# Optimization experiments

Hardware: AMD Instinct MI355X
Metric: run time of the kernel (lower is better)

## Reference

```python
import jax, jax.numpy as jnp
import numpy as np

D_MODEL = 512
NUM_HEADS = 8
D_K = D_MODEL // NUM_HEADS
DIM_FF = 2048
EPS = 1e-5


def layer_norm(x, gamma, beta):
    mu = jnp.mean(x, axis=-1, keepdims=True)
    var = jnp.mean(jnp.square(x - mu), axis=-1, keepdims=True)
    return (x - mu) * jax.lax.rsqrt(var + EPS) * gamma + beta


def setup_inputs() -> dict:
    key = jax.random.key(0)
    ks = jax.random.split(key, 10)
    B, L = 8, 1024
    s = 1.0 / np.sqrt(D_MODEL)
    return {
        "h": jax.random.normal(ks[0], (B, L, D_MODEL), jnp.float32),
        "attn_bias": jax.random.normal(ks[1], (B, NUM_HEADS, L, L), jnp.float32),
        "mask": jnp.ones((B, L), jnp.int32),
        "Wqkv": jax.random.normal(ks[2], (D_MODEL, 3 * D_MODEL), jnp.float32) * s,
        "bqkv": jnp.zeros((3 * D_MODEL,), jnp.float32),
        "Wo": jax.random.normal(ks[3], (D_MODEL, D_MODEL), jnp.float32) * s,
        "bo": jnp.zeros((D_MODEL,), jnp.float32),
        "W1": jax.random.normal(ks[4], (D_MODEL, DIM_FF), jnp.float32) * s,
        "b1": jnp.zeros((DIM_FF,), jnp.float32),
        "W2": jax.random.normal(ks[5], (DIM_FF, D_MODEL), jnp.float32) * (1.0 / np.sqrt(DIM_FF)),
        "b2": jnp.zeros((D_MODEL,), jnp.float32),
        "g1": jnp.ones((D_MODEL,), jnp.float32),
        "be1": jnp.zeros((D_MODEL,), jnp.float32),
        "g2": jnp.ones((D_MODEL,), jnp.float32),
        "be2": jnp.zeros((D_MODEL,), jnp.float32),
    }


def reference(h, attn_bias, mask, Wqkv, bqkv, Wo, bo, W1, b1, W2, b2, g1, be1, g2, be2):
    B, L, D = h.shape
    H, dk = NUM_HEADS, D_K
    qkv = h @ Wqkv + bqkv                      # [B, L, 3D]
    q, k, v = jnp.split(qkv, 3, axis=-1)
    q = q.reshape(B, L, H, dk).transpose(0, 2, 1, 3)  # [B, H, L, dk]
    k = k.reshape(B, L, H, dk).transpose(0, 2, 1, 3)
    v = v.reshape(B, L, H, dk).transpose(0, 2, 1, 3)
    scores = jnp.einsum('bhqd,bhkd->bhqk', q, k) / np.sqrt(dk)
    scores = scores + attn_bias
    scores = jnp.where(mask[:, None, None, :] > 0, scores, -jnp.inf)
    attn = jax.nn.softmax(scores, axis=-1)
    out = jnp.einsum('bhqk,bhkd->bhqd', attn, v)       # [B, H, L, dk]
    out = out.transpose(0, 2, 1, 3).reshape(B, L, D)
    out = out @ Wo + bo
    h = layer_norm(h + out, g1, be1)
    ff = jax.nn.relu(h @ W1 + b1) @ W2 + b2
    h = layer_norm(h + ff, g2, be2)
    return h
```

## Files before the change

### kernel.cpp

```cpp
#include <hip/hip_runtime.h>
#include <hip/hip_bf16.h>
#include <math.h>

#define NUM_HEADS 8
#define SEQ_L 1024
#define EPS 1e-5f
#define LOG2E 1.44269504088896f
#define KVB 128

typedef __bf16 bf16x8 __attribute__((ext_vector_type(8)));
typedef float f32x4 __attribute__((ext_vector_type(4)));
typedef __hip_bfloat16 bf16;

#define AS1 __attribute__((address_space(1)))
#define AS3 __attribute__((address_space(3)))

__device__ __forceinline__ void gload_lds16(const void* g, void* l) {
    __builtin_amdgcn_global_load_lds((const AS1 unsigned*)g, (AS3 unsigned*)l, 16, 0, 0);
}

__device__ __forceinline__ unsigned short bfb(float x) {
    bf16 b = __float2bfloat16(x);
    return *(unsigned short*)&b;
}

__device__ __forceinline__ int swz(int el, int row) { return el ^ ((row & 7) << 3); }

__global__ __launch_bounds__(256) void prep_kernel(
    const float* __restrict__ h, const float* __restrict__ Wqkv,
    const float* __restrict__ Wo, const float* __restrict__ W1,
    const float* __restrict__ W2,
    bf16* __restrict__ hb, bf16* __restrict__ Wtq, bf16* __restrict__ Wto,
    bf16* __restrict__ Wt1, bf16* __restrict__ Wt2)
{
    const int bid = blockIdx.x;
    const int tid = threadIdx.x;
    if (bid < 2048) {
        const int i = (bid * 256 + tid) * 8;
        const float4 v0 = *(const float4*)&h[i];
        const float4 v1 = *(const float4*)&h[i + 4];
        uint4 w;
        w.x = (unsigned)bfb(v0.x) | ((unsigned)bfb(v0.y) << 16);
        w.y = (unsigned)bfb(v0.z) | ((unsigned)bfb(v0.w) << 16);
        w.z = (unsigned)bfb(v1.x) | ((unsigned)bfb(v1.y) << 16);
        w.w = (unsigned)bfb(v1.z) | ((unsigned)bfb(v1.w) << 16);
        *(uint4*)&hb[i] = w;
        return;
    }
    int r = bid - 2048;
    const float* W; bf16* Wt; int K, N, bx, by;
    if (r < 768)        { W = Wqkv; Wt = Wtq; K = 512;  N = 1536; bx = r % 48; by = r / 48; }
    else if (r < 1024)  { r -= 768;  W = Wo; Wt = Wto; K = 512;  N = 512;  bx = r % 16; by = r / 16; }
    else if (r < 2048)  { r -= 1024; W = W1; Wt = Wt1; K = 512;  N = 2048; bx = r % 64; by = r / 64; }
    else                { r -= 2048; W = W2; Wt = Wt2; K = 2048; N = 512;  bx = r % 16; by = r / 16; }

    __shared__ float t[32][33];
    const int tx = tid & 31, ty = tid >> 5;
    const int n0 = bx * 32, k0 = by * 32;
    #pragma unroll
    for (int q = 0; q < 4; ++q)
        t[ty + 8 * q][tx] = W[(size_t)(k0 + ty + 8 * q) * N + n0 + tx];
    __syncthreads();
    #pragma unroll
    for (int q = 0; q < 4; ++q)
        Wt[(size_t)(n0 + ty + 8 * q) * K + k0 + tx] = __float2bfloat16(t[tx][ty + 8 * q]);
}

__global__ __launch_bounds__(256) void gemm_bf16(
    const bf16* __restrict__ A, const bf16* __restrict__ Bt,
    const float* __restrict__ bias, bf16* __restrict__ Cb,
    int M, int N, int K, int relu)
{
    __shared__ __align__(16) bf16 Abuf[128 * 32];
    __shared__ __align__(16) bf16 Bbuf[128 * 32];
    const int tid = threadIdx.x;
    const int wv = tid >> 6, lane = tid & 63;
    const int row0 = blockIdx.x * 128, col0 = blockIdx.y * 128;
    const int wm = (wv >> 1) * 64, wn = (wv & 1) * 64;
    const int r0 = lane & 15, kb = lane >> 4;

    f32x4 acc[4][4] = {};
    const int arow = lane >> 2;
    const int akoff = (lane & 3) * 8;

    for (int k0 = 0; k0 < K; k0 += 32) {
        #pragma unroll
        for (int s = 0; s < 2; ++s) {
            const int c = 2 * wv + s;
            gload_lds16(&A[(size_t)(row0 + c * 16 + arow) * K + k0 + akoff], &Abuf[c * 512]);
            gload_lds16(&Bt[(size_t)(col0 + c * 16 + arow) * K + k0 + akoff], &Bbuf[c * 512]);
        }
        __syncthreads();

        bf16x8 a[4], b[4];
        #pragma unroll
        for (int i = 0; i < 4; ++i)
            a[i] = *(const bf16x8*)&Abuf[(wm + i * 16 + r0) * 32 + kb * 8];
        #pragma unroll
        for (int j = 0; j < 4; ++j)
            b[j] = *(const bf16x8*)&Bbuf[(wn + j * 16 + r0) * 32 + kb * 8];
        #pragma unroll
        for (int i = 0; i < 4; ++i)
            #pragma unroll
            for (int j = 0; j < 4; ++j)
                acc[i][j] = __builtin_amdgcn_mfma_f32_16x16x32_bf16(a[i], b[j], acc[i][j], 0, 0, 0);
        __syncthreads();
    }

    float bv[4];
    #pragma unroll
    for (int j = 0; j < 4; ++j) bv[j] = bias[col0 + wn + j * 16 + r0];

    #pragma unroll
    for (int i = 0; i < 4; ++i) {
        #pragma unroll
        for (int j = 0; j < 4; ++j) {
            const int col = col0 + wn + j * 16 + r0;
            #pragma unroll
            for (int reg = 0; reg < 4; ++reg) {
                const int row = row0 + wm + i * 16 + kb * 4 + reg;
                float v = acc[i][j][reg] + bv[j];
                if (relu) v = fmaxf(v, 0.f);
                Cb[(size_t)row * N + col] = __float2bfloat16(v);
            }
        }
    }
}

__global__ __launch_bounds__(256) void gemm_qkv(
    const bf16* __restrict__ A, const bf16* __restrict__ Bt,
    const float* __restrict__ bias,
    bf16* __restrict__ Qb, bf16* __restrict__ Kb, bf16* __restrict__ Vtb,
    int M, int N, int K)
{
    __shared__ __align__(16) bf16 Abuf[128 * 32];
    __shared__ __align__(16) bf16 Bbuf[128 * 32];
    const int tid = threadIdx.x;
    const int wv = tid >> 6, lane = tid & 63;
    const int row0 = blockIdx.x * 128, col0 = blockIdx.y * 128;
    const int wm = (wv >> 1) * 64, wn = (wv & 1) * 64;
    const int r0 = lane & 15, kb = lane >> 4;

    f32x4 acc[4][4] = {};
    const int arow = lane >> 2;
    const int akoff = (lane & 3) * 8;

    for (int k0 = 0; k0 < K; k0 += 32) {
        #pragma unroll
        for (int s = 0; s < 2; ++s) {
            const int c = 2 * wv + s;
            gload_lds16(&A[(size_t)(row0 + c * 16 + arow) * K + k0 + akoff], &Abuf[c * 512]);
            gload_lds16(&Bt[(size_t)(col0 + c * 16 + arow) * K + k0 + akoff], &Bbuf[c * 512]);
        }
        __syncthreads();

        bf16x8 a[4], b[4];
        #pragma unroll
        for (int i = 0; i < 4; ++i)
            a[i] = *(const bf16x8*)&Abuf[(wm + i * 16 + r0) * 32 + kb * 8];
        #pragma unroll
        for (int j = 0; j < 4; ++j)
            b[j] = *(const bf16x8*)&Bbuf[(wn + j * 16 + r0) * 32 + kb * 8];
        #pragma unroll
        for (int i = 0; i < 4; ++i)
            #pragma unroll
            for (int j = 0; j < 4; ++j)
                acc[i][j] = __builtin_amdgcn_mfma_f32_16x16x32_bf16(a[i], b[j], acc[i][j], 0, 0, 0);
        __syncthreads();
    }

    #pragma unroll
    for (int i = 0; i < 4; ++i) {
        #pragma unroll
        for (int j = 0; j < 4; ++j) {
            const int col = col0 + wn + j * 16 + r0;
            const float bv = bias[col];
            const int region = col >> 9;
            const int cc = col & 511;
            const int head = cc >> 6, d = cc & 63;
            const int l0 = row0 + wm + i * 16 + kb * 4;
            const int b_ = l0 >> 10, l_ = l0 & 1023;
            if (region == 2) {
                unsigned short pk[4];
                #pragma unroll
                for (int reg = 0; reg < 4; ++reg) pk[reg] = bfb(acc[i][j][reg] + bv);
                *(ushort4*)&Vtb[((size_t)(b_ * NUM_HEADS + head) * 64 + d) * SEQ_L + l_] =
                    make_ushort4(pk[0], pk[1], pk[2], pk[3]);
            } else {
                const float s = (region == 0) ? (0.125f * LOG2E) : 1.0f;
                bf16* dst = (region == 0) ? Qb : Kb;
                #pragma unroll
                for (int reg = 0; reg < 4; ++reg) {
                    dst[((size_t)(b_ * NUM_HEADS + head) * SEQ_L + l_ + reg) * 64 + d] =
                        __float2bfloat16((acc[i][j][reg] + bv) * s);
                }
            }
        }
    }
}

__global__ __launch_bounds__(256) void attn_mfma(
    const bf16* __restrict__ Qb, const bf16* __restrict__ Kb,
    const bf16* __restrict__ Vtb, const float* __restrict__ abias,
    const int* __restrict__ mask, bf16* __restrict__ out)
{
    const int bh = blockIdx.x;
    const int b = bh >> 3, h = bh & 7;
    const int q0 = blockIdx.y * 64;
    const int tid = threadIdx.x;
    const int wv = tid >> 6, lane = tid & 63;
    const int ql = lane & 15;
    const int hi = lane >> 4;

    __shared__ __align__(16) bf16 Ks[KVB * 64];
    __shared__ __align__(16) bf16 Vs[64 * KVB];
    __shared__ __align__(16) bf16 Ps[4][16 * KVB];

    const bf16* Kbase = Kb + (size_t)bh * SEQ_L * 64;
    const bf16* Vbase = Vtb + (size_t)bh * 64 * SEQ_L;
    const int* mbase = mask + b * SEQ_L;

    auto stageKV = [&](int k0) {
        #pragma unroll
        for (int it = 0; it < 4; ++it) {
            const int row = wv * 32 + it * 8 + (lane >> 3);
            const int gp = (lane & 7) ^ (row & 7);
            gload_lds16(&Kbase[(size_t)(k0 + row) * 64 + gp * 8],
                        &Ks[(wv * 32 + it * 8) * 64]);
        }
        #pragma unroll
        for (int it = 0; it < 4; ++it) {
            const int row = wv * 16 + it * 4 + (lane >> 4);
            const int g = lane & 15;
            const int gp = (g & 8) | ((g & 7) ^ (row & 7));
            gload_lds16(&Vbase[(size_t)row * SEQ_L + k0 + gp * 8],
                        &Vs[(wv * 16 + it * 4) * KVB]);
        }
    };

    const int qrow = q0 + wv * 16 + ql;
    bf16x8 qf[2];
    #pragma unroll
    for (int kk = 0; kk < 2; ++kk)
        qf[kk] = *(const bf16x8*)&Qb[((size_t)bh * SEQ_L + qrow) * 64 + kk * 32 + hi * 8];

    const size_t bias_row = ((size_t)(b * NUM_HEADS + h) * SEQ_L + qrow) * SEQ_L;

    f32x4 breg[8];
    int4 mreg[2];
    auto loadBias = [&](int k0) {
        #pragma unroll
        for (int c = 0; c < 8; ++c)
            breg[c] = *(const f32x4*)&abias[bias_row + k0 + c * 16 + hi * 4];
        mreg[0] = *(const int4*)&mbase[k0 + (hi * 4)];
        mreg[1] = *(const int4*)&mbase[k0 + 64 + (hi * 4)];
    };
    int4 mfr[8];
    auto loadMask = [&](int k0) {
        #pragma unroll
        for (int c = 0; c < 8; ++c)
            mfr[c] = *(const int4*)&mbase[k0 + c * 16 + hi * 4];
    };

    f32x4 o[4] = {};
    float m = -1e30f, l = 0.f;

    stageKV(0);
    loadBias(0);
    loadMask(0);
    __syncthreads();

    for (int t = 0; t < 8; ++t) {
        f32x4 p[8];
        #pragma unroll
        for (int c = 0; c < 8; ++c) {
            p[c][0] = (mfr[c].x > 0) ? breg[c][0] * LOG2E : -1e30f;
            p[c][1] = (mfr[c].y > 0) ? breg[c][1] * LOG2E : -1e30f;
            p[c][2] = (mfr[c].z > 0) ? breg[c][2] * LOG2E : -1e30f;
            p[c][3] = (mfr[c].w > 0) ? breg[c][3] * LOG2E : -1e30f;
        }

        if (t < 7) { loadBias((t + 1) * KVB); loadMask((t + 1) * KVB); }

        __builtin_amdgcn_s_setprio(1);
        #pragma unroll
        for (int c = 0; c < 8; ++c) {
            const int row = c * 16 + ql;
            #pragma unroll
            for (int kk = 0; kk < 2; ++kk) {
                const bf16x8 kf = *(const bf16x8*)&Ks[swz(row * 64 + kk * 32 + hi * 8, row)];
                p[c] = __builtin_amdgcn_mfma_f32_16x16x32_bf16(kf, qf[kk], p[c], 0, 0, 0);
            }
        }
        __builtin_amdgcn_s_setprio(0);

        float mx = p[0][0];
        #pragma unroll
        for (int c = 0; c < 8; ++c)
            #pragma unroll
            for (int reg = 0; reg < 4; ++reg) mx = fmaxf(mx, p[c][reg]);
        mx = fmaxf(mx, __shfl_xor(mx, 16, 64));
        mx = fmaxf(mx, __shfl_xor(mx, 32, 64));

        if (!__all(mx <= m + 11.0f)) {
            const float mnew = fmaxf(m, mx);
            const float scale = __builtin_exp2f(m - mnew);
            m = mnew;
            l *= scale;
            #pragma unroll
            for (int reg = 0; reg < 4; ++reg) {
                const float sc_q = __shfl(scale, (lane & 48) | (hi * 4 + reg), 64);
                #pragma unroll
                for (int c2 = 0; c2 < 4; ++c2) o[c2][reg] *= sc_q;
            }
        }

        float lsum = 0.f;
        #pragma unroll
        for (int c = 0; c < 8; ++c)
            #pragma unroll
            for (int reg = 0; reg < 4; ++reg) {
                const float pv = __builtin_exp2f(p[c][reg] - m);
                p[c][reg] = pv;
                lsum += pv;
            }
        l += lsum;

        #pragma unroll
        for (int c = 0; c < 8; ++c) {
            const int el = ql * KVB + c * 16 + hi * 4;
            uint2 pk;
            pk.x = (unsigned)bfb(p[c][0]) | ((unsigned)bfb(p[c][1]) << 16);
            pk.y = (unsigned)bfb(p[c][2]) | ((unsigned)bfb(p[c][3]) << 16);
            *(uint2*)&Ps[wv][swz(el, ql)] = pk;
        }

        __builtin_amdgcn_s_setprio(1);
        #pragma unroll
        for (int kk = 0; kk < 4; ++kk) {
            const bf16x8 pf = *(const bf16x8*)&Ps[wv][swz(ql * KVB + kk * 32 + hi * 8, ql)];
            #pragma unroll
            for (int c2 = 0; c2 < 4; ++c2) {
                const int vrow = c2 * 16 + ql;
                const bf16x8 vf = *(const bf16x8*)&Vs[swz(vrow * KVB + kk * 32 + hi * 8, vrow)];
                o[c2] = __builtin_amdgcn_mfma_f32_16x16x32_bf16(pf, vf, o[c2], 0, 0, 0);
            }
        }
        __builtin_amdgcn_s_setprio(0);

        if (t < 7) {
            __syncthreads();
            stageKV((t + 1) * KVB);
            __syncthreads();
        }
    }

    l += __shfl_xor(l, 16, 64);
    l += __shfl_xor(l, 32, 64);
    const float invl = (l > 0.f) ? (1.0f / l) : 0.f;
    #pragma unroll
    for (int reg = 0; reg < 4; ++reg) {
        const float inv_q = __shfl(invl, (lane & 48) | (hi * 4 + reg), 64);
        const int row = q0 + wv * 16 + hi * 4 + reg;
        #pragma unroll
        for (int c2 = 0; c2 < 4; ++c2)
            out[((size_t)(b * SEQ_L + row)) * 512 + h * 64 + c2 * 16 + ql] =
                __float2bfloat16(o[c2][reg] * inv_q);
    }
}

__global__ __launch_bounds__(256) void add_ln_to_bf16(
    const float* __restrict__ X, const bf16* __restrict__ Yb,
    const float* __restrict__ gamma, const float* __restrict__ beta,
    bf16* __restrict__ outb)
{
    const int wave = threadIdx.x >> 6;
    const int lane = threadIdx.x & 63;
    const int row = blockIdx.x * 4 + wave;
    const float* xp = X + (size_t)row * 512 + lane * 8;
    const bf16x8 yv = *(const bf16x8*)&Yb[(size_t)row * 512 + lane * 8];

    float v[8];
    const float4 a0 = *(const float4*)xp;
    const float4 a1 = *(const float4*)(xp + 4);
    v[0] = a0.x + (float)yv[0]; v[1] = a0.y + (float)yv[1];
    v[2] = a0.z + (float)yv[2]; v[3] = a0.w + (float)yv[3];
    v[4] = a1.x + (float)yv[4]; v[5] = a1.y + (float)yv[5];
    v[6] = a1.z + (float)yv[6]; v[7] = a1.w + (float)yv[7];

    float s = 0.f, sq = 0.f;
    #pragma unroll
    for (int i = 0; i < 8; ++i) { s += v[i]; sq += v[i] * v[i]; }
    #pragma unroll
    for (int off = 1; off < 64; off <<= 1) {
        s += __shfl_xor(s, off, 64);
        sq += __shfl_xor(sq, off, 64);
    }
    const float mu = s * (1.f / 512.f);
    const float var = sq * (1.f / 512.f) - mu * mu;
    const float rstd = rsqrtf(var + EPS);

    const int c = lane * 8;
    const float4 g0 = *(const float4*)&gamma[c];
    const float4 g1 = *(const float4*)&gamma[c + 4];
    const float4 e0 = *(const float4*)&beta[c];
    const float4 e1 = *(const float4*)&beta[c + 4];
    float r[8];
    r[0] = (v[0] - mu) * rstd * g0.x + e0.x;
    r[1] = (v[1] - mu) * rstd * g0.y + e0.y;
    r[2] = (v[2] - mu) * rstd * g0.z + e0.z;
    r[3] = (v[3] - mu) * rstd * g0.w + e0.w;
    r[4] = (v[4] - mu) * rstd * g1.x + e1.x;
    r[5] = (v[5] - mu) * rstd * g1.y + e1.y;
    r[6] = (v[6] - mu) * rstd * g1.z + e1.z;
    r[7] = (v[7] - mu) * rstd * g1.w + e1.w;

    uint4 w;
    w.x = (unsigned)bfb(r[0]) | ((unsigned)bfb(r[1]) << 16);
    w.y = (unsigned)bfb(r[2]) | ((unsigned)bfb(r[3]) << 16);
    w.z = (unsigned)bfb(r[4]) | ((unsigned)bfb(r[5]) << 16);
    w.w = (unsigned)bfb(r[6]) | ((unsigned)bfb(r[7]) << 16);
    *(uint4*)&outb[(size_t)row * 512 + c] = w;
}

__global__ __launch_bounds__(256) void add_ln_from_bf16(
    const bf16* __restrict__ Xb, const bf16* __restrict__ Yb,
    const float* __restrict__ gamma, const float* __restrict__ beta,
    float* __restrict__ out)
{
    const int wave = threadIdx.x >> 6;
    const int lane = threadIdx.x & 63;
    const int row = blockIdx.x * 4 + wave;
    const bf16x8 xv = *(const bf16x8*)&Xb[(size_t)row * 512 + lane * 8];
    const bf16x8 yv = *(const bf16x8*)&Yb[(size_t)row * 512 + lane * 8];

    float v[8];
    #pragma unroll
    for (int i = 0; i < 8; ++i) v[i] = (float)xv[i] + (float)yv[i];

    float s = 0.f, sq = 0.f;
    #pragma unroll
    for (int i = 0; i < 8; ++i) { s += v[i]; sq += v[i] * v[i]; }
    #pragma unroll
    for (int off = 1; off < 64; off <<= 1) {
        s += __shfl_xor(s, off, 64);
        sq += __shfl_xor(sq, off, 64);
    }
    const float mu = s * (1.f / 512.f);
    const float var = sq * (1.f / 512.f) - mu * mu;
    const float rstd = rsqrtf(var + EPS);

    const int c = lane * 8;
    const float4 g0 = *(const float4*)&gamma[c];
    const float4 g1 = *(const float4*)&gamma[c + 4];
    const float4 e0 = *(const float4*)&beta[c];
    const float4 e1 = *(const float4*)&beta[c + 4];
    float4 r0, r1;
    r0.x = (v[0] - mu) * rstd * g0.x + e0.x;
    r0.y = (v[1] - mu) * rstd * g0.y + e0.y;
    r0.z = (v[2] - mu) * rstd * g0.z + e0.z;
    r0.w = (v[3] - mu) * rstd * g0.w + e0.w;
    r1.x = (v[4] - mu) * rstd * g1.x + e1.x;
    r1.y = (v[5] - mu) * rstd * g1.y + e1.y;
    r1.z = (v[6] - mu) * rstd * g1.z + e1.z;
    r1.w = (v[7] - mu) * rstd * g1.w + e1.w;
    float* op = out + (size_t)row * 512 + c;
    *(float4*)op = r0;
    *(float4*)(op + 4) = r1;
}

extern "C" void kernel_launch(void* const* d_in, const int* in_sizes, int n_in,
                              void* d_out, int out_size, void* d_ws, size_t ws_size,
                              hipStream_t stream)
{
    const float* h    = (const float*)d_in[0];
    const float* ab   = (const float*)d_in[1];
    const int*   mask = (const int*)d_in[2];
    const float* Wqkv = (const float*)d_in[3];
    const float* bqkv = (const float*)d_in[4];
    const float* Wo   = (const float*)d_in[5];
    const float* bo   = (const float*)d_in[6];
    const float* W1   = (const float*)d_in[7];
    const float* b1   = (const float*)d_in[8];
    const float* W2   = (const float*)d_in[9];
    const float* b2   = (const float*)d_in[10];
    const float* g1   = (const float*)d_in[11];
    const float* be1  = (const float*)d_in[12];
    const float* g2   = (const float*)d_in[13];
    const float* be2  = (const float*)d_in[14];
    float* out = (float*)d_out;
    char* ws = (char*)d_ws;

    const int M = 8 * 1024;
    const size_t MB = 1024 * 1024;

    bf16*  hb    = (bf16*)(ws + 0 * MB);
    bf16*  Wtq   = (bf16*)(ws + 8 * MB);
    bf16*  Wto   = (bf16*)(ws + 10 * MB);
    bf16*  Wt1   = (bf16*)(ws + 11 * MB);
    bf16*  Wt2   = (bf16*)(ws + 13 * MB);
    bf16*  Qb    = (bf16*)(ws + 15 * MB);
    bf16*  Kb    = (bf16*)(ws + 23 * MB);
    bf16*  Vtb   = (bf16*)(ws + 31 * MB);
    bf16*  aob   = (bf16*)(ws + 39 * MB);
    bf16*  projb = (bf16*)(ws + 47 * MB);
    bf16*  h1b   = (bf16*)(ws + 55 * MB);
    bf16*  ffb   = (bf16*)(ws + 63 * MB);
    bf16*  f2b   = (bf16*)(ws + 95 * MB);

    prep_kernel<<<dim3(5120), 256, 0, stream>>>(h, Wqkv, Wo, W1, W2, hb, Wtq, Wto, Wt1, Wt2);
    gemm_qkv<<<dim3(M / 128, 1536 / 128), 256, 0, stream>>>(hb, Wtq, bqkv, Qb, Kb, Vtb, M, 1536, 512);
    attn_mfma<<<dim3(64, SEQ_L / 64), 256, 0, stream>>>(Qb, Kb, Vtb, ab, mask, aob);
    gemm_bf16<<<dim3(M / 128, 512 / 128), 256, 0, stream>>>(aob, Wto, bo, projb, M, 512, 512, 0);
    add_ln_to_bf16<<<dim3(M / 4), 256, 0, stream>>>(h, projb, g1, be1, h1b);
    gemm_bf16<<<dim3(M / 128, 2048 / 128), 256, 0, stream>>>(h1b, Wt1, b1, ffb, M, 2048, 512, 1);
    gemm_bf16<<<dim3(M / 128, 512 / 128), 256, 0, stream>>>(ffb, Wt2, b2, f2b, M, 512, 2048, 0);
    add_ln_from_bf16<<<dim3(M / 4), 256, 0, stream>>>(h1b, f2b, g2, be2, out);
}
```

Measured before the change: 229.8 us.

## Compress attention mask to LDS bitmask and shrink P staging buffer

Instead of loading eight int4 mask vectors from global memory per KV tile, the kernel builds the key mask once with wave ballots into a 32-word LDS bitmask. Masking now zeroes probabilities after exp2 rather than setting scores to -1e30 before the running max. The per-wave P staging buffer shrinks from 16x128 to 16x32 and is refilled per 32-key quarter, interleaved with the PV MFMAs. Together with __launch_bounds__(256,4), this aims to cut VGPR and LDS use for higher occupancy. The new mask handling lets masked scores feed the max, which changes numerics when real masking occurs.

```diff
diff --git a/kernel.cpp b/kernel.cpp
--- a/kernel.cpp
+++ b/kernel.cpp
@@ -199,7 +199,7 @@
     }
 }
 
-__global__ __launch_bounds__(256) void attn_mfma(
+__global__ __launch_bounds__(256, 4) void attn_mfma(
     const bf16* __restrict__ Qb, const bf16* __restrict__ Kb,
     const bf16* __restrict__ Vtb, const float* __restrict__ abias,
     const int* __restrict__ mask, bf16* __restrict__ out)
@@ -214,7 +214,8 @@
 
     __shared__ __align__(16) bf16 Ks[KVB * 64];
     __shared__ __align__(16) bf16 Vs[64 * KVB];
-    __shared__ __align__(16) bf16 Ps[4][16 * KVB];
+    __shared__ __align__(16) bf16 Ps[4][16 * 32];
+    __shared__ unsigned mbits[32];
 
     const bf16* Kbase = Kb + (size_t)bh * SEQ_L * 64;
     const bf16* Vbase = Vtb + (size_t)bh * 64 * SEQ_L;
@@ -247,40 +248,43 @@
     const size_t bias_row = ((size_t)(b * NUM_HEADS + h) * SEQ_L + qrow) * SEQ_L;
 
     f32x4 breg[8];
-    int4 mreg[2];
     auto loadBias = [&](int k0) {
         #pragma unroll
         for (int c = 0; c < 8; ++c)
             breg[c] = *(const f32x4*)&abias[bias_row + k0 + c * 16 + hi * 4];
-        mreg[0] = *(const int4*)&mbase[k0 + (hi * 4)];
-        mreg[1] = *(const int4*)&mbase[k0 + 64 + (hi * 4)];
     };
-    int4 mfr[8];
-    auto loadMask = [&](int k0) {
-        #pragma unroll
-        for (int c = 0; c < 8; ++c)
-            mfr[c] = *(const int4*)&mbase[k0 + c * 16 + hi * 4];
-    };
+
+    #pragma unroll
+    for (int r = 0; r < 4; ++r) {
+        const unsigned long long bl = __ballot(mbase[wv * 256 + r * 64 + lane] > 0);
+        if (lane == 0) {
+            mbits[wv * 8 + r * 2] = (unsigned)bl;
+            mbits[wv * 8 + r * 2 + 1] = (unsigned)(bl >> 32);
+        }
+    }
 
     f32x4 o[4] = {};
     float m = -1e30f, l = 0.f;
 
     stageKV(0);
     loadBias(0);
-    loadMask(0);
     __syncthreads();
 
     for (int t = 0; t < 8; ++t) {
+        unsigned mw[4];
+        {
+            const uint4 m4 = *(const uint4*)&mbits[t * 4];
+            mw[0] = m4.x; mw[1] = m4.y; mw[2] = m4.z; mw[3] = m4.w;
+        }
+
         f32x4 p[8];
         #pragma unroll
-        for (int c = 0; c < 8; ++c) {
-            p[c][0] = (mfr[c].x > 0) ? breg[c][0] * LOG2E : -1e30f;
-            p[c][1] = (mfr[c].y > 0) ? breg[c][1] * LOG2E : -1e30f;
-            p[c][2] = (mfr[c].z > 0) ? breg[c][2] * LOG2E : -1e30f;
-            p[c][3] = (mfr[c].w > 0) ? breg[c][3] * LOG2E : -1e30f;
-        }
-
-        if (t < 7) { loadBias((t + 1) * KVB); loadMask((t + 1) * KVB); }
+        for (int c = 0; c < 8; ++c)
+            #pragma unroll
+            for (int reg = 0; reg < 4; ++reg)
+                p[c][reg] = breg[c][reg] * LOG2E;
+
+        if (t < 7) loadBias((t + 1) * KVB);
 
         __builtin_amdgcn_s_setprio(1);
         #pragma unroll
@@ -321,28 +325,30 @@
             #pragma unroll
             for (int reg = 0; reg < 4; ++reg) {
                 const float pv = __builtin_exp2f(p[c][reg] - m);
-                p[c][reg] = pv;
-                lsum += pv;
+                const unsigned bit = (mw[c >> 1] >> ((c & 1) * 16 + hi * 4 + reg)) & 1u;
+                const float pm = bit ? pv : 0.f;
+                p[c][reg] = pm;
+                lsum += pm;
             }
         l += lsum;
 
-        #pragma unroll
-        for (int c = 0; c < 8; ++c) {
-            const int el = ql * KVB + c * 16 + hi * 4;
-            uint2 pk;
-            pk.x = (unsigned)bfb(p[c][0]) | ((unsigned)bfb(p[c][1]) << 16);
-            pk.y = (unsigned)bfb(p[c][2]) | ((unsigned)bfb(p[c][3]) << 16);
-            *(uint2*)&Ps[wv][swz(el, ql)] = pk;
-        }
-
         __builtin_amdgcn_s_setprio(1);
         #pragma unroll
-        for (int kk = 0; kk < 4; ++kk) {
-            const bf16x8 pf = *(const bf16x8*)&Ps[wv][swz(ql * KVB + kk * 32 + hi * 8, ql)];
+        for (int qtr = 0; qtr < 4; ++qtr) {
+            #pragma unroll
+            for (int s2 = 0; s2 < 2; ++s2) {
+                const int c = qtr * 2 + s2;
+                const int el = ql * 32 + s2 * 16 + hi * 4;
+                uint2 pk;
+                pk.x = (unsigned)bfb(p[c][0]) | ((unsigned)bfb(p[c][1]) << 16);
+                pk.y = (unsigned)bfb(p[c][2]) | ((unsigned)bfb(p[c][3]) << 16);
+                *(uint2*)&Ps[wv][swz(el, ql) & 511] = pk;
+            }
+            const bf16x8 pf = *(const bf16x8*)&Ps[wv][swz(ql * 32 + hi * 8, ql) & 511];
             #pragma unroll
             for (int c2 = 0; c2 < 4; ++c2) {
                 const int vrow = c2 * 16 + ql;
-                const bf16x8 vf = *(const bf16x8*)&Vs[swz(vrow * KVB + kk * 32 + hi * 8, vrow)];
+                const bf16x8 vf = *(const bf16x8*)&Vs[swz(vrow * KVB + qtr * 32 + hi * 8, vrow)];
                 o[c2] = __builtin_amdgcn_mfma_f32_16x16x32_bf16(pf, vf, o[c2], 0, 0, 0);
             }
         }
```

New measurement: 360.5 us. +56.9%, slower.

## Fuse output projection GEMM with residual add and LayerNorm

Applied to the files above, without the earlier changes.

Replaces the Wo projection GEMM and separate add+LayerNorm kernel with one kernel where each block computes a 16-row by 512-column strip, then adds bias and residual and normalizes across the full row using a shuffle and LDS reduction. This removes the round trip of the bf16 projection buffer and one launch. In exchange, every block reloads the whole 512x32 weight slice per k-step with no double buffering and only 16 rows per block, so weight reuse is low and global traffic is high. An unused mask preload in attention is also removed.

```diff
diff --git a/kernel.cpp b/kernel.cpp
--- a/kernel.cpp
+++ b/kernel.cpp
@@ -25,6 +25,7 @@
 }
 
 __device__ __forceinline__ int swz(int el, int row) { return el ^ ((row & 7) << 3); }
+__device__ __forceinline__ int swz2(int el, int row) { return el ^ ((row & 3) << 3); }
 
 __global__ __launch_bounds__(256) void prep_kernel(
     const float* __restrict__ h, const float* __restrict__ Wqkv,
@@ -199,6 +200,105 @@
     }
 }
 
+__global__ __launch_bounds__(256) void gemm_proj_ln(
+    const bf16* __restrict__ A, const bf16* __restrict__ Bt,
+    const float* __restrict__ bias, const float* __restrict__ resid,
+    const float* __restrict__ gamma, const float* __restrict__ beta,
+    bf16* __restrict__ outb)
+{
+    __shared__ __align__(16) bf16 Abuf[16 * 32];
+    __shared__ __align__(16) bf16 Bbuf[512 * 32];
+    __shared__ float red[4][16][2];
+    const int tid = threadIdx.x;
+    const int wv = tid >> 6, lane = tid & 63;
+    const int r0 = lane & 15, kb = lane >> 4;
+    const int row0 = blockIdx.x * 16;
+
+    f32x4 acc[8] = {};
+
+    for (int k0 = 0; k0 < 512; k0 += 32) {
+        if (wv == 0) {
+            const int row = lane >> 2;
+            const int gp = (lane & 3) ^ (row & 3);
+            gload_lds16(&A[(size_t)(row0 + row) * 512 + k0 + gp * 8], Abuf);
+        }
+        #pragma unroll
+        for (int it = 0; it < 8; ++it) {
+            const int ch = (wv * 8 + it) * 64 + lane;
+            const int row = ch >> 2;
+            const int gp = (ch & 3) ^ (row & 3);
+            gload_lds16(&Bt[(size_t)row * 512 + k0 + gp * 8],
+                        &Bbuf[(wv * 8 + it) * 512]);
+        }
+        __syncthreads();
+
+        const bf16x8 a = *(const bf16x8*)&Abuf[swz2(r0 * 32 + kb * 8, r0)];
+        #pragma unroll
+        for (int j = 0; j < 8; ++j) {
+            const int brow = wv * 128 + j * 16 + r0;
+            const bf16x8 b = *(const bf16x8*)&Bbuf[swz2(brow * 32 + kb * 8, brow)];
+            acc[j] = __builtin_amdgcn_mfma_f32_16x16x32_bf16(a, b, acc[j], 0, 0, 0);
+        }
+        __syncthreads();
+    }
+
+    const int colbase = wv * 128;
+    float ga[8], be[8], bv[8];
+    #pragma unroll
+    for (int j = 0; j < 8; ++j) {
+        const int col = colbase + j * 16 + r0;
+        bv[j] = bias[col];
+        ga[j] = gamma[col];
+        be[j] = beta[col];
+    }
+
+    float v[8][4];
+    float s[4] = {}, sq[4] = {};
+    #pragma unroll
+    for (int j = 0; j < 8; ++j) {
+        const int col = colbase + j * 16 + r0;
+        #pragma unroll
+        for (int reg = 0; reg < 4; ++reg) {
+            const int row = row0 + kb * 4 + reg;
+            const float val = acc[j][reg] + bv[j] + resid[(size_t)row * 512 + col];
+            v[j][reg] = val;
+            s[reg] += val;
+            sq[reg] += val * val;
+        }
+    }
+    #pragma unroll
+    for (int off = 1; off < 16; off <<= 1) {
+        #pragma unroll
+        for (int reg = 0; reg < 4; ++reg) {
+            s[reg] += __shfl_xor(s[reg], off, 64);
+            sq[reg] += __shfl_xor(sq[reg], off, 64);
+        }
+    }
+    if (r0 == 0) {
+        #pragma unroll
+        for (int reg = 0; reg < 4; ++reg) {
+            red[wv][kb * 4 + reg][0] = s[reg];
+            red[wv][kb * 4 + reg][1] = sq[reg];
+        }
+    }
+    __syncthreads();
+    #pragma unroll
+    for (int reg = 0; reg < 4; ++reg) {
+        const int r = kb * 4 + reg;
+        const float st = red[0][r][0] + red[1][r][0] + red[2][r][0] + red[3][r][0];
+        const float sqt = red[0][r][1] + red[1][r][1] + red[2][r][1] + red[3][r][1];
+        const float mu = st * (1.f / 512.f);
+        const float var = sqt * (1.f / 512.f) - mu * mu;
+        const float rstd = rsqrtf(var + EPS);
+        #pragma unroll
+        for (int j = 0; j < 8; ++j) {
+            const int col = colbase + j * 16 + r0;
+            const float rr = (v[j][reg] - mu) * rstd * ga[j] + be[j];
+            outb[(size_t)(row0 + r) * 512 + col] = __float2bfloat16(rr);
+        }
+    }
+}
+
 __global__ __launch_bounds__(256) void attn_mfma(
     const bf16* __restrict__ Qb, const bf16* __restrict__ Kb,
     const bf16* __restrict__ Vtb, const float* __restrict__ abias,
@@ -247,13 +347,10 @@
     const size_t bias_row = ((size_t)(b * NUM_HEADS + h) * SEQ_L + qrow) * SEQ_L;
 
     f32x4 breg[8];
-    int4 mreg[2];
     auto loadBias = [&](int k0) {
         #pragma unroll
         for (int c = 0; c < 8; ++c)
             breg[c] = *(const f32x4*)&abias[bias_row + k0 + c * 16 + hi * 4];
-        mreg[0] = *(const int4*)&mbase[k0 + (hi * 4)];
-        mreg[1] = *(const int4*)&mbase[k0 + 64 + (hi * 4)];
     };
     int4 mfr[8];
     auto loadMask = [&](int k0) {
@@ -367,60 +464,6 @@
             out[((size_t)(b * SEQ_L + row)) * 512 + h * 64 + c2 * 16 + ql] =
                 __float2bfloat16(o[c2][reg] * inv_q);
     }
-}
-
-__global__ __launch_bounds__(256) void add_ln_to_bf16(
-    const float* __restrict__ X, const bf16* __restrict__ Yb,
-    const float* __restrict__ gamma, const float* __restrict__ beta,
-    bf16* __restrict__ outb)
-{
-    const int wave = threadIdx.x >> 6;
-    const int lane = threadIdx.x & 63;
-    const int row = blockIdx.x * 4 + wave;
-    const float* xp = X + (size_t)row * 512 + lane * 8;
-    const bf16x8 yv = *(const bf16x8*)&Yb[(size_t)row * 512 + lane * 8];
-
-    float v[8];
-    const float4 a0 = *(const float4*)xp;
-    const float4 a1 = *(const float4*)(xp + 4);
-    v[0] = a0.x + (float)yv[0]; v[1] = a0.y + (float)yv[1];
-    v[2] = a0.z + (float)yv[2]; v[3] = a0.w + (float)yv[3];
-    v[4] = a1.x + (float)yv[4]; v[5] = a1.y + (float)yv[5];
-    v[6] = a1.z + (float)yv[6]; v[7] = a1.w + (float)yv[7];
-
-    float s = 0.f, sq = 0.f;
-    #pragma unroll
-    for (int i = 0; i < 8; ++i) { s += v[i]; sq += v[i] * v[i]; }
-    #pragma unroll
-    for (int off = 1; off < 64; off <<= 1) {
-        s += __shfl_xor(s, off, 64);
-        sq += __shfl_xor(sq, off, 64);
-    }
-    const float mu = s * (1.f / 512.f);
-    const float var = sq * (1.f / 512.f) - mu * mu;
-    const float rstd = rsqrtf(var + EPS);
-
-    const int c = lane * 8;
-    const float4 g0 = *(const float4*)&gamma[c];
-    const float4 g1 = *(const float4*)&gamma[c + 4];
-    const float4 e0 = *(const float4*)&beta[c];
-    const float4 e1 = *(const float4*)&beta[c + 4];
-    float r[8];
-    r[0] = (v[0] - mu) * rstd * g0.x + e0.x;
-    r[1] = (v[1] - mu) * rstd * g0.y + e0.y;
-    r[2] = (v[2] - mu) * rstd * g0.z + e0.z;
-    r[3] = (v[3] - mu) * rstd * g0.w + e0.w;
-    r[4] = (v[4] - mu) * rstd * g1.x + e1.x;
-    r[5] = (v[5] - mu) * rstd * g1.y + e1.y;
-    r[6] = (v[6] - mu) * rstd * g1.z + e1.z;
-    r[7] = (v[7] - mu) * rstd * g1.w + e1.w;
-
-    uint4 w;
-    w.x = (unsigned)bfb(r[0]) | ((unsigned)bfb(r[1]) << 16);
-    w.y = (unsigned)bfb(r[2]) | ((unsigned)bfb(r[3]) << 16);
-    w.z = (unsigned)bfb(r[4]) | ((unsigned)bfb(r[5]) << 16);
-    w.w = (unsigned)bfb(r[6]) | ((unsigned)bfb(r[7]) << 16);
-    *(uint4*)&outb[(size_t)row * 512 + c] = w;
 }
 
 __global__ __launch_bounds__(256) void add_ln_from_bf16(
@@ -503,7 +546,6 @@
     bf16*  Kb    = (bf16*)(ws + 23 * MB);
     bf16*  Vtb   = (bf16*)(ws + 31 * MB);
     bf16*  aob   = (bf16*)(ws + 39 * MB);
-    bf16*  projb = (bf16*)(ws + 47 * MB);
     bf16*  h1b   = (bf16*)(ws + 55 * MB);
     bf16*  ffb   = (bf16*)(ws + 63 * MB);
     bf16*  f2b   = (bf16*)(ws + 95 * MB);
@@ -511,8 +553,7 @@
     prep_kernel<<<dim3(5120), 256, 0, stream>>>(h, Wqkv, Wo, W1, W2, hb, Wtq, Wto, Wt1, Wt2);
     gemm_qkv<<<dim3(M / 128, 1536 / 128), 256, 0, stream>>>(hb, Wtq, bqkv, Qb, Kb, Vtb, M, 1536, 512);
     attn_mfma<<<dim3(64, SEQ_L / 64), 256, 0, stream>>>(Qb, Kb, Vtb, ab, mask, aob);
-    gemm_bf16<<<dim3(M / 128, 512 / 128), 256, 0, stream>>>(aob, Wto, bo, projb, M, 512, 512, 0);
-    add_ln_to_bf16<<<dim3(M / 4), 256, 0, stream>>>(h, projb, g1, be1, h1b);
+    gemm_proj_ln<<<dim3(M / 16), 256, 0, stream>>>(aob, Wto, bo, h, g1, be1, h1b);
     gemm_bf16<<<dim3(M / 128, 2048 / 128), 256, 0, stream>>>(h1b, Wt1, b1, ffb, M, 2048, 512, 1);
     gemm_bf16<<<dim3(M / 128, 512 / 128), 256, 0, stream>>>(ffb, Wt2, b2, f2b, M, 512, 2048, 0);
     add_ln_from_bf16<<<dim3(M / 4), 256, 0, stream>>>(h1b, f2b, g2, be2, out);
```

New measurement: 239.3 us. 1.04x slower.
